# Optimization experiments

Measured on AMD Instinct MI355X. Metric: run time of the kernel, lower is better.

The kernel has to match this reference:

```python
import jax, jax.numpy as jnp
import numpy as np

B, D, A, H, NH = 32768, 768, 17, 128, 4
DH = H // NH


def _ln(x, g, b, eps=1e-5):
    mu = jnp.mean(x, axis=-1, keepdims=True)
    var = jnp.mean((x - mu) ** 2, axis=-1, keepdims=True)
    return (x - mu) / jnp.sqrt(var + eps) * g + b


def setup_inputs() -> dict:
    key = jax.random.key(0)
    ks = jax.random.split(key, 16)
    s = 0.02
    return {
        "visual_feat": jax.random.normal(ks[0], (B, D), jnp.float32),
        "au_feat": jax.random.uniform(ks[1], (B, A), jnp.float32),
        "w_tok": jax.random.normal(ks[2], (H, 1), jnp.float32) * s,
        "b_tok": jnp.zeros((H,), jnp.float32),
        "pos": jax.random.normal(ks[3], (1, A, H), jnp.float32) * s,
        "g_auln": jnp.ones((H,), jnp.float32),
        "b_auln": jnp.zeros((H,), jnp.float32),
        "w_q": jax.random.normal(ks[4], (H, D), jnp.float32) * s,
        "b_q": jnp.zeros((H,), jnp.float32),
        "w_in": jax.random.normal(ks[5], (3 * H, H), jnp.float32) * s,  # packed q,k,v in_proj
        "b_in": jnp.zeros((3 * H,), jnp.float32),
        "w_ao": jax.random.normal(ks[6], (H, H), jnp.float32) * s,  # MHA out_proj
        "b_ao": jnp.zeros((H,), jnp.float32),
        "g_aln": jnp.ones((H,), jnp.float32),
        "b_aln": jnp.zeros((H,), jnp.float32),
        "w_out": jax.random.normal(ks[7], (D, H), jnp.float32) * s,
        "b_out": jnp.zeros((D,), jnp.float32),
        "w_gate": jax.random.normal(ks[8], (D, 2 * D), jnp.float32) * s,
        "b_gate": jnp.zeros((D,), jnp.float32),
    }


def reference(visual_feat, au_feat, w_tok, b_tok, pos, g_auln, b_auln,
              w_q, b_q, w_in, b_in, w_ao, b_ao, g_aln, b_aln,
              w_out, b_out, w_gate, b_gate):
    # AU tokens: Linear(1 -> H) on intensities, + pos embed, LN. [B, A, H]
    au_tokens = au_feat[..., None] * w_tok[:, 0] + b_tok
    au_tokens = _ln(au_tokens + pos, g_auln, b_auln)
    # query: [B, H] (seq len 1)
    query = visual_feat @ w_q.T + b_q
    # MultiheadAttention (batch_first, packed in_proj)
    wq, wk, wv = w_in[:H], w_in[H:2 * H], w_in[2 * H:]
    bq, bk, bv = b_in[:H], b_in[H:2 * H], b_in[2 * H:]
    q = (query @ wq.T + bq).reshape(-1, NH, DH)          # [B, nh, dh]
    k = (au_tokens @ wk.T + bk).reshape(-1, A, NH, DH)   # [B, A, nh, dh]
    v = (au_tokens @ wv.T + bv).reshape(-1, A, NH, DH)
    scale = 1.0 / jnp.sqrt(jnp.asarray(DH, q.dtype))
    scores = jnp.einsum('bhd,bahd->bha', q * scale, k)   # [B, nh, A]
    attn = jax.nn.softmax(scores, axis=-1)
    ctx = jnp.einsum('bha,bahd->bhd', attn, v).reshape(-1, H)
    attn_out = ctx @ w_ao.T + b_ao
    attn_out = _ln(attn_out, g_aln, b_aln)
    attn_feat = attn_out @ w_out.T + b_out               # [B, D]
    gate_in = jnp.concatenate([visual_feat, attn_feat], axis=1)
    gate = jax.nn.sigmoid(gate_in @ w_gate.T + b_gate)
    return gate * attn_feat + (1.0 - gate) * visual_feat
```

## Files before the change

### kernel.cpp

```cpp
#include <hip/hip_runtime.h>
#include <hip/hip_bf16.h>

typedef __hip_bfloat16 bf16;
typedef __attribute__((ext_vector_type(8))) short short8;
typedef __attribute__((ext_vector_type(4))) float f32x4;
typedef __attribute__((ext_vector_type(8))) __bf16 bf16x8;

#define NB 32768
#define DD 768
#define AA 17
#define HH 128

__device__ __forceinline__ float bs2f(short s){
  unsigned int u = ((unsigned int)(unsigned short)s) << 16;
  return __builtin_bit_cast(float, u);
}
__device__ __forceinline__ short f2bs(float f){
  bf16 h = __float2bfloat16(f);
  return __builtin_bit_cast(short, h);
}
__device__ __forceinline__ f32x4 mfma16(short8 a, short8 b, f32x4 c){
  return __builtin_amdgcn_mfma_f32_16x16x32_bf16(
      __builtin_bit_cast(bf16x8, a), __builtin_bit_cast(bf16x8, b), c, 0, 0, 0);
}

template<int F32>
__device__ __forceinline__ short8 ldchunk(const void* base, long elem_off){
  if (F32){
    const float4* p = (const float4*)((const float*)base + elem_off);
    float4 x = p[0], y = p[1];
    short8 r;
    r[0]=f2bs(x.x); r[1]=f2bs(x.y); r[2]=f2bs(x.z); r[3]=f2bs(x.w);
    r[4]=f2bs(y.x); r[5]=f2bs(y.y); r[6]=f2bs(y.z); r[7]=f2bs(y.w);
    return r;
  } else {
    return *(const short8*)((const short*)base + elem_off);
  }
}


__device__ __forceinline__ float blk_mean128(float v, float* tmp){
  int t = threadIdx.x;
  #pragma unroll
  for (int m = 32; m; m >>= 1) v += __shfl_xor(v, m);
  if ((t & 63) == 0) tmp[t >> 6] = v;
  __syncthreads();
  float r = (tmp[0] + tmp[1]) * (1.0f / 128.0f);
  __syncthreads();
  return r;
}

__global__ void prep1(const float* __restrict__ w_tok, const float* __restrict__ b_tok,
                      const float* __restrict__ pos, const float* __restrict__ g_auln,
                      float* __restrict__ ug, float* __restrict__ rg, float* __restrict__ coef){
  __shared__ float tmp[2];
  int h = threadIdx.x;
  float w = w_tok[h];
  float wbar = blk_mean128(w, tmp);
  float u = w - wbar;
  float g = g_auln[h];
  ug[h] = u * g;
  float muu = blk_mean128(u * u, tmp);
  if (h == 0) coef[0] = muu;
  float bt = b_tok[h];
  for (int a = 0; a < AA; ++a){
    float c = bt + pos[a * HH + h];
    float cbar = blk_mean128(c, tmp);
    float r = c - cbar;
    rg[a * HH + h] = r * g;
    float mur = blk_mean128(u * r, tmp);
    float mrr = blk_mean128(r * r, tmp);
    if (h == 0){ coef[1 + a] = mur; coef[18 + a] = mrr; }
  }
}

__global__ void prep2(const float* __restrict__ w_in, const float* __restrict__ b_in,
                      const float* __restrict__ b_auln, const float* __restrict__ b_q,
                      const float* __restrict__ ug, const float* __restrict__ rg,
                      float* __restrict__ Uk, float* __restrict__ Ck,
                      float* __restrict__ Uv, float* __restrict__ Cv,
                      float* __restrict__ Rk, float* __restrict__ Rv,
                      float* __restrict__ bqf){
  int hp = threadIdx.x, bid = blockIdx.x;
  const float* wqrow = w_in + (long)hp * HH;
  const float* wkrow = w_in + (long)(HH + hp) * HH;
  const float* wvrow = w_in + (long)(2 * HH + hp) * HH;
  if (bid < AA){
    int a = bid;
    float sk = 0.f, sv = 0.f;
    for (int t = 0; t < HH; ++t){
      float r = rg[a * HH + t];
      sk += r * wkrow[t];
      sv += r * wvrow[t];
    }
    Rk[a * HH + hp] = sk; Rv[a * HH + hp] = sv;
  } else if (bid == AA){
    float uk = 0.f, uv = 0.f, ck = 0.f, cv = 0.f;
    for (int t = 0; t < HH; ++t){
      float u = ug[t], ba = b_auln[t];
      float wk = wkrow[t], wv = wvrow[t];
      uk += u * wk; uv += u * wv; ck += ba * wk; cv += ba * wv;
    }
    Uk[hp] = uk; Uv[hp] = uv;
    Ck[hp] = ck + b_in[HH + hp];
    Cv[hp] = cv + b_in[2 * HH + hp];
  } else {
    float s = 0.f;
    for (int t = 0; t < HH; ++t) s += b_q[t] * wqrow[t];
    bqf[hp] = s + b_in[hp];
  }
}

__global__ void prep_wqf(const float* __restrict__ w_in, const float* __restrict__ w_q,
                         bf16* __restrict__ Wqf){
  __shared__ float wq[HH];
  int h = blockIdx.x, t = threadIdx.x;
  if (t < HH) wq[t] = w_in[(long)h * HH + t];
  __syncthreads();
  for (int j = t; j < DD; j += 256){
    float acc = 0.f;
    for (int k = 0; k < HH; ++k) acc += wq[k] * w_q[(long)k * DD + j];
    Wqf[(long)h * DD + j] = __float2bfloat16(acc);
  }
}

__global__ void prep_gate(const float* __restrict__ w_gate, const float* __restrict__ b_gate,
                          const float* __restrict__ w_out, const float* __restrict__ b_out,
                          bf16* __restrict__ Wg1b, bf16* __restrict__ Wg2w,
                          bf16* __restrict__ Woutb, float* __restrict__ bgp){
  __shared__ float wg2[DD];
  __shared__ float red[2];
  int c = blockIdx.x, t = threadIdx.x;
  const float* wrow = w_gate + (long)c * (2 * DD);
  for (int j = t; j < DD; j += 128){
    Wg1b[(long)c * DD + j] = __float2bfloat16(wrow[j]);
    wg2[j] = wrow[DD + j];
  }
  __syncthreads();
  float acc = 0.f;
  for (int j = 0; j < DD; ++j) acc = fmaf(wg2[j], w_out[(long)j * HH + t], acc);
  Wg2w[(long)c * HH + t] = __float2bfloat16(acc);
  Woutb[(long)c * HH + t] = __float2bfloat16(w_out[(long)c * HH + t]);
  float pb = 0.f;
  for (int j = t; j < DD; j += 128) pb = fmaf(wg2[j], b_out[j], pb);
  #pragma unroll
  for (int m = 32; m; m >>= 1) pb += __shfl_xor(pb, m);
  if ((t & 63) == 0) red[t >> 6] = pb;
  __syncthreads();
  if (t == 0) bgp[c] = b_gate[c] + red[0] + red[1];
}

__global__ __launch_bounds__(128) void attn(
    const bf16* __restrict__ Q, const float* __restrict__ au, const float* __restrict__ coef,
    const float* __restrict__ Uk_, const float* __restrict__ Ck_,
    const float* __restrict__ Uv_, const float* __restrict__ Cv_,
    const float* __restrict__ Rk, const float* __restrict__ Rv,
    bf16* __restrict__ ctx){
  const int ROWS = 8;
  int h = threadIdx.x;
  long row0 = (long)blockIdx.x * ROWS;
  float Uk = Uk_[h], Ck = Ck_[h], Uv = Uv_[h], Cv = Cv_[h];
  float cA = coef[0];
  __shared__ float sa[ROWS * AA];
  for (int idx = h; idx < ROWS * AA; idx += 128)
    sa[idx] = au[row0 * AA + idx];
  __syncthreads();
  const float scale = 0.17677669529663689f;
  for (int r = 0; r < ROWS; ++r){
    long row = row0 + r;
    float q = __bfloat162float(Q[row * HH + h]);
    float sc[AA], vv[AA];
    #pragma unroll
    for (int a = 0; a < AA; ++a){
      float s = sa[r * AA + a];
      float var = fmaf(s * s, cA, fmaf(2.f * s, coef[1 + a], coef[18 + a]));
      float rinv = rsqrtf(fmaxf(var, 0.f) + 1e-5f);
      float kk = fmaf(s, Uk, Rk[a * HH + h]) * rinv + Ck;
      vv[a]    = fmaf(s, Uv, Rv[a * HH + h]) * rinv + Cv;
      float p = q * kk;
      p += __shfl_xor(p, 16); p += __shfl_xor(p, 8); p += __shfl_xor(p, 4);
      p += __shfl_xor(p, 2);  p += __shfl_xor(p, 1);
      sc[a] = p * scale;
    }
    float mx = sc[0];
    #pragma unroll
    for (int a = 1; a < AA; ++a) mx = fmaxf(mx, sc[a]);
    float den = 0.f, cval = 0.f;
    #pragma unroll
    for (int a = 0; a < AA; ++a){
      float e = __expf(sc[a] - mx);
      den += e; cval += e * vv[a];
    }
    ctx[row * HH + h] = __float2bfloat16(cval / den);
  }
}

template<int MODE, int AF, int BF, int SIDE>
__global__ __launch_bounds__(256) void gemm_bt(
    const void* __restrict__ A, long lda, int ks,
    const void* __restrict__ Bw, long ldb,
    const float* __restrict__ bias,
    const float* __restrict__ g_ln, const float* __restrict__ b_ln,
    short* __restrict__ sideA,
    bf16* __restrict__ C, long ldc)
{
  __shared__ __align__(16) short smem[20480];
  const int tid = threadIdx.x;
  const int w = tid >> 6, l = tid & 63;
  const long rowBase = (long)blockIdx.y * 128;
  const int colBase = blockIdx.x * 128;
  const int fr = l & 15;
  const int kq = l >> 4;
  const int sr0 = tid >> 2,         sp0 = (tid & 3) * 8;
  const int sr1 = (tid + 256) >> 2;

  f32x4 acc[2][8];
  f32x4 zero = {0.f, 0.f, 0.f, 0.f};
  #pragma unroll
  for (int i = 0; i < 2; ++i)
    #pragma unroll
    for (int j = 0; j < 8; ++j) acc[i][j] = zero;

  {
    short8 av0 = ldchunk<AF>(A, (rowBase + sr0) * lda + sp0);
    short8 av1 = ldchunk<AF>(A, (rowBase + sr1) * lda + sp0);
    short8 bv0 = ldchunk<BF>(Bw, (long)(colBase + sr0) * ldb + sp0);
    short8 bv1 = ldchunk<BF>(Bw, (long)(colBase + sr1) * ldb + sp0);
    if (SIDE){
      *(short8*)(sideA + (rowBase + sr0) * lda + sp0) = av0;
      *(short8*)(sideA + (rowBase + sr1) * lda + sp0) = av1;
    }
    *(short8*)(smem + sr0 * 40 + sp0) = av0;
    *(short8*)(smem + sr1 * 40 + sp0) = av1;
    *(short8*)(smem + 5120 + sr0 * 40 + sp0) = bv0;
    *(short8*)(smem + 5120 + sr1 * 40 + sp0) = bv1;
  }

  for (int kt = 0; kt < ks; ++kt){
    __syncthreads();
    short* cb = smem + (kt & 1) * 10240;
    short* nb = smem + ((kt + 1) & 1) * 10240;
    const bool pf = (kt + 1 < ks);
    short8 av0, av1, bv0, bv1;
    if (pf){
      const long kA = (long)(kt + 1) * 32;
      av0 = ldchunk<AF>(A, (rowBase + sr0) * lda + kA + sp0);
      av1 = ldchunk<AF>(A, (rowBase + sr1) * lda + kA + sp0);
      bv0 = ldchunk<BF>(Bw, (long)(colBase + sr0) * ldb + kA + sp0);
      bv1 = ldchunk<BF>(Bw, (long)(colBase + sr1) * ldb + kA + sp0);
      if (SIDE){
        *(short8*)(sideA + (rowBase + sr0) * lda + kA + sp0) = av0;
        *(short8*)(sideA + (rowBase + sr1) * lda + kA + sp0) = av1;
      }
    }
    const int ra0 = w * 32 + fr;
    short8 a0 = *(const short8*)(cb + ra0 * 40 + kq * 8);
    short8 a1 = *(const short8*)(cb + (ra0 + 16) * 40 + kq * 8);
    #pragma unroll
    for (int nt = 0; nt < 8; ++nt){
      short8 b = *(const short8*)(cb + 5120 + (nt * 16 + fr) * 40 + kq * 8);
      acc[0][nt] = mfma16(a0, b, acc[0][nt]);
      acc[1][nt] = mfma16(a1, b, acc[1][nt]);
    }
    if (pf){
      *(short8*)(nb + sr0 * 40 + sp0) = av0;
      *(short8*)(nb + sr1 * 40 + sp0) = av1;
      *(short8*)(nb + 5120 + sr0 * 40 + sp0) = bv0;
      *(short8*)(nb + 5120 + sr1 * 40 + sp0) = bv1;
    }
  }
  __syncthreads();

  short* ep = smem;
  if (MODE == 1){
    #pragma unroll
    for (int mt = 0; mt < 2; ++mt){
      #pragma unroll
      for (int r = 0; r < 4; ++r){
        float x[8]; float sm = 0.f, sq = 0.f;
        #pragma unroll
        for (int nt = 0; nt < 8; ++nt){
          const int col = colBase + nt * 16 + fr;
          x[nt] = acc[mt][nt][r] + bias[col];
          sm += x[nt]; sq += x[nt] * x[nt];
        }
        sm += __shfl_xor(sm, 1); sq += __shfl_xor(sq, 1);
        sm += __shfl_xor(sm, 2); sq += __shfl_xor(sq, 2);
        sm += __shfl_xor(sm, 4); sq += __shfl_xor(sq, 4);
        sm += __shfl_xor(sm, 8); sq += __shfl_xor(sq, 8);
        const float mu = sm * (1.f / 128.f);
        const float var = sq * (1.f / 128.f) - mu * mu;
        const float rinv = rsqrtf(fmaxf(var, 0.f) + 1e-5f);
        const int lrow = w * 32 + mt * 16 + kq * 4 + r;
        #pragma unroll
        for (int nt = 0; nt < 8; ++nt){
          const int col = colBase + nt * 16 + fr;
          float y = (x[nt] - mu) * rinv * g_ln[col] + b_ln[col];
          ep[lrow * 136 + nt * 16 + fr] = f2bs(y);
        }
      }
    }
  } else {
    #pragma unroll
    for (int nt = 0; nt < 8; ++nt){
      const int col = colBase + nt * 16 + fr;
      const float bv = bias[col];
      #pragma unroll
      for (int mt = 0; mt < 2; ++mt){
        const int lrow0 = w * 32 + mt * 16 + kq * 4;
        #pragma unroll
        for (int r = 0; r < 4; ++r)
          ep[(lrow0 + r) * 136 + nt * 16 + fr] = f2bs(acc[mt][nt][r] + bv);
      }
    }
  }
  __syncthreads();

  #pragma unroll
  for (int it = 0; it < 8; ++it){
    const int cid = tid + it * 256;
    const int rw = cid >> 4;
    const int cc = (cid & 15) * 8;
    const long gr = rowBase + rw;
    short8 vls = *(const short8*)(ep + rw * 136 + cc);
    short* cp = (short*)C + gr * ldc + colBase + cc;
    *(short8*)cp = vls;
  }
}

template<int A1F>
__global__ __launch_bounds__(256) void gemm_final(
    const void* __restrict__ A1,
    const bf16* __restrict__ aon,
    const bf16* __restrict__ Wg1b,
    const bf16* __restrict__ Wg2w,
    const bf16* __restrict__ Woutb,
    const float* __restrict__ bgp,
    const float* __restrict__ b_out,
    const float* __restrict__ vf,
    float* __restrict__ C)
{
  __shared__ __align__(16) short smem[20480];
  const int tid = threadIdx.x;
  const int w = tid >> 6, l = tid & 63;

  const int nx = 6;
  const int bid = blockIdx.y * nx + blockIdx.x;
  const int cpx = (NB / 128) * nx / 8;
  const int swz = (bid & 7) * cpx + (bid >> 3);
  const long rowBase = (long)(swz / nx) * 128;
  const int colBase = (swz % nx) * 128;

  const int fr = l & 15;
  const int kq = l >> 4;
  const int sr0 = tid >> 2,         sp0 = (tid & 3) * 8;
  const int sr1 = (tid + 256) >> 2;

  f32x4 accG[2][8], accF[2][8];
  f32x4 zero = {0.f, 0.f, 0.f, 0.f};
  #pragma unroll
  for (int i = 0; i < 2; ++i)
    #pragma unroll
    for (int j = 0; j < 8; ++j){ accG[i][j] = zero; accF[i][j] = zero; }

  {
    short8 av0 = ldchunk<A1F>(A1, (rowBase + sr0) * DD + sp0);
    short8 av1 = ldchunk<A1F>(A1, (rowBase + sr1) * DD + sp0);
    short8 bv0 = *(const short8*)((const short*)Wg1b + (long)(colBase + sr0) * DD + sp0);
    short8 bv1 = *(const short8*)((const short*)Wg1b + (long)(colBase + sr1) * DD + sp0);
    *(short8*)(smem + sr0 * 40 + sp0) = av0;
    *(short8*)(smem + sr1 * 40 + sp0) = av1;
    *(short8*)(smem + 5120 + sr0 * 40 + sp0) = bv0;
    *(short8*)(smem + 5120 + sr1 * 40 + sp0) = bv1;
  }
  for (int kt = 0; kt < DD / 32; ++kt){
    __syncthreads();
    short* cb = smem + (kt & 1) * 10240;
    short* nb = smem + ((kt + 1) & 1) * 10240;
    const bool pf = (kt + 1 < DD / 32);
    short8 av0, av1, bv0, bv1;
    if (pf){
      const long kA = (long)(kt + 1) * 32;
      av0 = ldchunk<A1F>(A1, (rowBase + sr0) * DD + kA + sp0);
      av1 = ldchunk<A1F>(A1, (rowBase + sr1) * DD + kA + sp0);
      bv0 = *(const short8*)((const short*)Wg1b + (long)(colBase + sr0) * DD + kA + sp0);
      bv1 = *(const short8*)((const short*)Wg1b + (long)(colBase + sr1) * DD + kA + sp0);
    }
    const int ra0 = w * 32 + fr;
    short8 a0 = *(const short8*)(cb + ra0 * 40 + kq * 8);
    short8 a1 = *(const short8*)(cb + (ra0 + 16) * 40 + kq * 8);
    #pragma unroll
    for (int nt = 0; nt < 8; ++nt){
      short8 b = *(const short8*)(cb + 5120 + (nt * 16 + fr) * 40 + kq * 8);
      accG[0][nt] = mfma16(a0, b, accG[0][nt]);
      accG[1][nt] = mfma16(a1, b, accG[1][nt]);
    }
    if (pf){
      *(short8*)(nb + sr0 * 40 + sp0) = av0;
      *(short8*)(nb + sr1 * 40 + sp0) = av1;
      *(short8*)(nb + 5120 + sr0 * 40 + sp0) = bv0;
      *(short8*)(nb + 5120 + sr1 * 40 + sp0) = bv1;
    }
  }

  short* As = smem;
  short* Bs = smem + 5120;
  short* Bs2 = smem + 10240;
  for (int kt = 0; kt < HH / 32; ++kt){
    const long kA = (long)kt * 32;
    short8 av0 = *(const short8*)((const short*)aon + (rowBase + sr0) * HH + kA + sp0);
    short8 av1 = *(const short8*)((const short*)aon + (rowBase + sr1) * HH + kA + sp0);
    short8 bv0 = *(const short8*)((const short*)Wg2w + (long)(colBase + sr0) * HH + kA + sp0);
    short8 bv1 = *(const short8*)((const short*)Wg2w + (long)(colBase + sr1) * HH + kA + sp0);
    short8 cv0 = *(const short8*)((const short*)Woutb + (long)(colBase + sr0) * HH + kA + sp0);
    short8 cv1 = *(const short8*)((const short*)Woutb + (long)(colBase + sr1) * HH + kA + sp0);
    __syncthreads();
    *(short8*)(As + sr0 * 40 + sp0) = av0;
    *(short8*)(As + sr1 * 40 + sp0) = av1;
    *(short8*)(Bs + sr0 * 40 + sp0) = bv0;
    *(short8*)(Bs + sr1 * 40 + sp0) = bv1;
    *(short8*)(Bs2 + sr0 * 40 + sp0) = cv0;
    *(short8*)(Bs2 + sr1 * 40 + sp0) = cv1;
    __syncthreads();
    const int ra0 = w * 32 + fr;
    short8 a0 = *(const short8*)(As + ra0 * 40 + kq * 8);
    short8 a1 = *(const short8*)(As + (ra0 + 16) * 40 + kq * 8);
    #pragma unroll
    for (int nt = 0; nt < 8; ++nt){
      short8 b  = *(const short8*)(Bs  + (nt * 16 + fr) * 40 + kq * 8);
      short8 b2 = *(const short8*)(Bs2 + (nt * 16 + fr) * 40 + kq * 8);
      accG[0][nt] = mfma16(a0, b,  accG[0][nt]);
      accG[1][nt] = mfma16(a1, b,  accG[1][nt]);
      accF[0][nt] = mfma16(a0, b2, accF[0][nt]);
      accF[1][nt] = mfma16(a1, b2, accF[1][nt]);
    }
  }

  float bg[8], bo[8];
  #pragma unroll
  for (int nt = 0; nt < 8; ++nt){
    const int col = colBase + nt * 16 + fr;
    bg[nt] = bgp[col];
    bo[nt] = b_out[col];
  }
  #pragma unroll
  for (int mt = 0; mt < 2; ++mt){
    const long r0 = rowBase + w * 32 + mt * 16 + kq * 4;
    #pragma unroll
    for (int r = 0; r < 4; ++r){
      const long row = r0 + r;
      const float* vrow = vf + row * DD;
      float* crow = C + row * DD;
      #pragma unroll
      for (int nt = 0; nt < 8; ++nt){
        const int col = colBase + nt * 16 + fr;
        const float lin = accG[mt][nt][r] + bg[nt];
        const float afv = accF[mt][nt][r] + bo[nt];
        const float gate = 1.f / (1.f + __expf(-lin));
        crow[col] = gate * afv + (1.f - gate) * vrow[col];
      }
    }
  }
}

extern "C" void kernel_launch(void* const* d_in, const int* in_sizes, int n_in,
                              void* d_out, int out_size, void* d_ws, size_t ws_size,
                              hipStream_t stream){
  const float* visual = (const float*)d_in[0];
  const float* au     = (const float*)d_in[1];
  const float* w_tok  = (const float*)d_in[2];
  const float* b_tok  = (const float*)d_in[3];
  const float* pos    = (const float*)d_in[4];
  const float* g_auln = (const float*)d_in[5];
  const float* b_auln = (const float*)d_in[6];
  const float* w_q    = (const float*)d_in[7];
  const float* b_q    = (const float*)d_in[8];
  const float* w_in   = (const float*)d_in[9];
  const float* b_in   = (const float*)d_in[10];
  const float* w_ao   = (const float*)d_in[11];
  const float* b_ao   = (const float*)d_in[12];
  const float* g_aln  = (const float*)d_in[13];
  const float* b_aln  = (const float*)d_in[14];
  const float* w_out  = (const float*)d_in[15];
  const float* b_out  = (const float*)d_in[16];
  const float* w_gate = (const float*)d_in[17];
  const float* b_gate = (const float*)d_in[18];

  char* ob = (char*)d_out;
  bf16* Q   = (bf16*)(ob);
  bf16* ctx = (bf16*)(ob + ((size_t)8 << 20));
  char* p = ob + ((size_t)16 << 20);
  auto alloc = [&](size_t bytes){ char* r = p; p += (bytes + 255) & ~(size_t)255; return r; };
  bf16*  Wqf  = (bf16*) alloc((size_t)HH * DD * 2);
  float* bqf  = (float*)alloc(HH * 4);
  float* ug   = (float*)alloc(HH * 4);
  float* rg   = (float*)alloc(AA * HH * 4);
  float* coef = (float*)alloc(64 * 4);
  float* Uk   = (float*)alloc(HH * 4);
  float* Ck   = (float*)alloc(HH * 4);
  float* Uv   = (float*)alloc(HH * 4);
  float* Cv   = (float*)alloc(HH * 4);
  float* Rk   = (float*)alloc(AA * HH * 4);
  float* Rv   = (float*)alloc(AA * HH * 4);

  char* q = (char*)d_ws;
  auto walloc = [&](size_t bytes){ char* r = q; q += (bytes + 255) & ~(size_t)255; return r; };
  bf16*  aon   = (bf16*) walloc((size_t)NB * HH * 2);
  bf16*  Wg1b  = (bf16*) walloc((size_t)DD * DD * 2);
  bf16*  Wg2w  = (bf16*) walloc((size_t)DD * HH * 2);
  bf16*  Woutb = (bf16*) walloc((size_t)DD * HH * 2);
  float* bgp   = (float*)walloc(DD * 4);
  bf16*  vbf   = (bf16*) walloc((size_t)NB * DD * 2);
  const bool use_vbf = (size_t)(q - (char*)d_ws) <= ws_size;

  prep1<<<dim3(1), dim3(128), 0, stream>>>(w_tok, b_tok, pos, g_auln, ug, rg, coef);
  prep2<<<dim3(19), dim3(128), 0, stream>>>(w_in, b_in, b_auln, b_q, ug, rg, Uk, Ck, Uv, Cv, Rk, Rv, bqf);
  prep_wqf<<<dim3(128), dim3(256), 0, stream>>>(w_in, w_q, Wqf);
  prep_gate<<<dim3(DD), dim3(128), 0, stream>>>(w_gate, b_gate, w_out, b_out, Wg1b, Wg2w, Woutb, bgp);

  if (use_vbf)
    gemm_bt<0, 1, 0, 1><<<dim3(1, NB / 128), dim3(256), 0, stream>>>(
        visual, (long)DD, DD / 32, Wqf, (long)DD,
        bqf, nullptr, nullptr, (short*)vbf, Q, (long)HH);
  else
    gemm_bt<0, 1, 0, 0><<<dim3(1, NB / 128), dim3(256), 0, stream>>>(
        visual, (long)DD, DD / 32, Wqf, (long)DD,
        bqf, nullptr, nullptr, nullptr, Q, (long)HH);

  attn<<<dim3(NB / 8), dim3(128), 0, stream>>>(Q, au, coef, Uk, Ck, Uv, Cv, Rk, Rv, ctx);

  gemm_bt<1, 0, 1, 0><<<dim3(1, NB / 128), dim3(256), 0, stream>>>(
      ctx, (long)HH, HH / 32, w_ao, (long)HH,
      b_ao, g_aln, b_aln, nullptr, aon, (long)HH);

  if (use_vbf)
    gemm_final<0><<<dim3(DD / 128, NB / 128), dim3(256), 0, stream>>>(
        vbf, aon, Wg1b, Wg2w, Woutb, bgp, b_out, visual, (float*)d_out);
  else
    gemm_final<1><<<dim3(DD / 128, NB / 128), dim3(256), 0, stream>>>(
        visual, aon, Wg1b, Wg2w, Woutb, bgp, b_out, visual, (float*)d_out);
}
```

Before: 578.0 us.

## Stage gate GEMM tiles via global_load_lds with XOR-swizzled shared layout

In the final gated GEMM, the bf16 path now loads A and weight tiles straight from global memory into LDS with global_load_lds, double-buffered. This drops the register round-trip and the padded layout, and an XOR swizzle on the 16-byte chunks is meant to avoid bank conflicts. The fp32-input path switches to a single-buffered swizzled layout. The intent is to cut VGPR pressure, instruction count and LDS usage, which may raise occupancy. The risk is that the async-copy synchronisation relies only on __syncthreads before the next tile is read.

```diff
diff --git a/kernel.cpp b/kernel.cpp
--- a/kernel.cpp
+++ b/kernel.cpp
@@ -5,6 +5,8 @@
 typedef __attribute__((ext_vector_type(8))) short short8;
 typedef __attribute__((ext_vector_type(4))) float f32x4;
 typedef __attribute__((ext_vector_type(8))) __bf16 bf16x8;
+typedef const __attribute__((address_space(1))) void* gas_ptr;
+typedef __attribute__((address_space(3))) void* las_ptr;
 
 #define NB 32768
 #define DD 768
@@ -22,6 +24,9 @@
 __device__ __forceinline__ f32x4 mfma16(short8 a, short8 b, f32x4 c){
   return __builtin_amdgcn_mfma_f32_16x16x32_bf16(
       __builtin_bit_cast(bf16x8, a), __builtin_bit_cast(bf16x8, b), c, 0, 0, 0);
+}
+__device__ __forceinline__ void glds16(const short* g, short* l){
+  __builtin_amdgcn_global_load_lds((gas_ptr)g, (las_ptr)l, 16, 0, 0);
 }
 
 template<int F32>
@@ -340,9 +345,9 @@
     const float* __restrict__ vf,
     float* __restrict__ C)
 {
-  __shared__ __align__(16) short smem[20480];
+  __shared__ __align__(16) short smem[16384];
   const int tid = threadIdx.x;
-  const int w = tid >> 6, l = tid & 63;
+  const int wv = tid >> 6, l = tid & 63;
 
   const int nx = 6;
   const int bid = blockIdx.y * nx + blockIdx.x;
@@ -353,8 +358,7 @@
 
   const int fr = l & 15;
   const int kq = l >> 4;
-  const int sr0 = tid >> 2,         sp0 = (tid & 3) * 8;
-  const int sr1 = (tid + 256) >> 2;
+  const int swofs = ((kq ^ ((l >> 1) & 3)) << 3);
 
   f32x4 accG[2][8], accF[2][8];
   f32x4 zero = {0.f, 0.f, 0.f, 0.f};
@@ -363,76 +367,102 @@
     #pragma unroll
     for (int j = 0; j < 8; ++j){ accG[i][j] = zero; accF[i][j] = zero; }
 
+  if (A1F == 0){
+    const short* Ab = (const short*)A1;
+    const short* Bb = (const short*)Wg1b;
+    const int srow = l >> 2;
+    const int schunk = ((l & 3) ^ ((l >> 3) & 3)) * 8;
+    #define STAGE_P1(p, kt) {                                                        \
+      short* dA = smem + (p) * 8192;                                                 \
+      _Pragma("unroll")                                                              \
+      for (int i = 0; i < 2; ++i){                                                   \
+        const int r = wv * 32 + i * 16 + srow;                                       \
+        glds16(Ab + ((rowBase + r) * (long)DD + (kt) * 32 + schunk),                 \
+               dA + wv * 1024 + i * 512);                                            \
+        glds16(Bb + ((long)(colBase + r) * DD + (kt) * 32 + schunk),                 \
+               dA + 4096 + wv * 1024 + i * 512);                                     \
+      }                                                                              \
+    }
+    STAGE_P1(0, 0);
+    for (int kt = 0; kt < DD / 32; ++kt){
+      __syncthreads();
+      if (kt + 1 < DD / 32) STAGE_P1((kt + 1) & 1, kt + 1);
+      short* cb = smem + (kt & 1) * 8192;
+      const int ra0 = wv * 32 + fr;
+      short8 a0 = *(const short8*)(cb + ra0 * 32 + swofs);
+      short8 a1 = *(const short8*)(cb + (ra0 + 16) * 32 + swofs);
+      #pragma unroll
+      for (int nt = 0; nt < 8; ++nt){
+        short8 b = *(const short8*)(cb + 4096 + (nt * 16 + fr) * 32 + swofs);
+        accG[0][nt] = mfma16(a0, b, accG[0][nt]);
+        accG[1][nt] = mfma16(a1, b, accG[1][nt]);
+      }
+    }
+    #undef STAGE_P1
+  } else {
+    const int sr0 = tid >> 2, sc = tid & 3;
+    const int sr1 = sr0 + 64;
+    const int sp = sc * 8;
+    const int ss0 = (sc ^ ((sr0 >> 1) & 3)) * 8;
+    const int ss1 = (sc ^ ((sr1 >> 1) & 3)) * 8;
+    for (int kt = 0; kt < DD / 32; ++kt){
+      const long kA = (long)kt * 32;
+      short8 av0 = ldchunk<1>(A1, (rowBase + sr0) * (long)DD + kA + sp);
+      short8 av1 = ldchunk<1>(A1, (rowBase + sr1) * (long)DD + kA + sp);
+      short8 bv0 = *(const short8*)((const short*)Wg1b + (long)(colBase + sr0) * DD + kA + sp);
+      short8 bv1 = *(const short8*)((const short*)Wg1b + (long)(colBase + sr1) * DD + kA + sp);
+      __syncthreads();
+      *(short8*)(smem + sr0 * 32 + ss0) = av0;
+      *(short8*)(smem + sr1 * 32 + ss1) = av1;
+      *(short8*)(smem + 4096 + sr0 * 32 + ss0) = bv0;
+      *(short8*)(smem + 4096 + sr1 * 32 + ss1) = bv1;
+      __syncthreads();
+      const int ra0 = wv * 32 + fr;
+      short8 a0 = *(const short8*)(smem + ra0 * 32 + swofs);
+      short8 a1 = *(const short8*)(smem + (ra0 + 16) * 32 + swofs);
+      #pragma unroll
+      for (int nt = 0; nt < 8; ++nt){
+        short8 b = *(const short8*)(smem + 4096 + (nt * 16 + fr) * 32 + swofs);
+        accG[0][nt] = mfma16(a0, b, accG[0][nt]);
+        accG[1][nt] = mfma16(a1, b, accG[1][nt]);
+      }
+    }
+  }
+
   {
-    short8 av0 = ldchunk<A1F>(A1, (rowBase + sr0) * DD + sp0);
-    short8 av1 = ldchunk<A1F>(A1, (rowBase + sr1) * DD + sp0);
-    short8 bv0 = *(const short8*)((const short*)Wg1b + (long)(colBase + sr0) * DD + sp0);
-    short8 bv1 = *(const short8*)((const short*)Wg1b + (long)(colBase + sr1) * DD + sp0);
-    *(short8*)(smem + sr0 * 40 + sp0) = av0;
-    *(short8*)(smem + sr1 * 40 + sp0) = av1;
-    *(short8*)(smem + 5120 + sr0 * 40 + sp0) = bv0;
-    *(short8*)(smem + 5120 + sr1 * 40 + sp0) = bv1;
-  }
-  for (int kt = 0; kt < DD / 32; ++kt){
-    __syncthreads();
-    short* cb = smem + (kt & 1) * 10240;
-    short* nb = smem + ((kt + 1) & 1) * 10240;
-    const bool pf = (kt + 1 < DD / 32);
-    short8 av0, av1, bv0, bv1;
-    if (pf){
-      const long kA = (long)(kt + 1) * 32;
-      av0 = ldchunk<A1F>(A1, (rowBase + sr0) * DD + kA + sp0);
-      av1 = ldchunk<A1F>(A1, (rowBase + sr1) * DD + kA + sp0);
-      bv0 = *(const short8*)((const short*)Wg1b + (long)(colBase + sr0) * DD + kA + sp0);
-      bv1 = *(const short8*)((const short*)Wg1b + (long)(colBase + sr1) * DD + kA + sp0);
-    }
-    const int ra0 = w * 32 + fr;
-    short8 a0 = *(const short8*)(cb + ra0 * 40 + kq * 8);
-    short8 a1 = *(const short8*)(cb + (ra0 + 16) * 40 + kq * 8);
-    #pragma unroll
-    for (int nt = 0; nt < 8; ++nt){
-      short8 b = *(const short8*)(cb + 5120 + (nt * 16 + fr) * 40 + kq * 8);
-      accG[0][nt] = mfma16(a0, b, accG[0][nt]);
-      accG[1][nt] = mfma16(a1, b, accG[1][nt]);
-    }
-    if (pf){
-      *(short8*)(nb + sr0 * 40 + sp0) = av0;
-      *(short8*)(nb + sr1 * 40 + sp0) = av1;
-      *(short8*)(nb + 5120 + sr0 * 40 + sp0) = bv0;
-      *(short8*)(nb + 5120 + sr1 * 40 + sp0) = bv1;
-    }
-  }
-
-  short* As = smem;
-  short* Bs = smem + 5120;
-  short* Bs2 = smem + 10240;
-  for (int kt = 0; kt < HH / 32; ++kt){
-    const long kA = (long)kt * 32;
-    short8 av0 = *(const short8*)((const short*)aon + (rowBase + sr0) * HH + kA + sp0);
-    short8 av1 = *(const short8*)((const short*)aon + (rowBase + sr1) * HH + kA + sp0);
-    short8 bv0 = *(const short8*)((const short*)Wg2w + (long)(colBase + sr0) * HH + kA + sp0);
-    short8 bv1 = *(const short8*)((const short*)Wg2w + (long)(colBase + sr1) * HH + kA + sp0);
-    short8 cv0 = *(const short8*)((const short*)Woutb + (long)(colBase + sr0) * HH + kA + sp0);
-    short8 cv1 = *(const short8*)((const short*)Woutb + (long)(colBase + sr1) * HH + kA + sp0);
-    __syncthreads();
-    *(short8*)(As + sr0 * 40 + sp0) = av0;
-    *(short8*)(As + sr1 * 40 + sp0) = av1;
-    *(short8*)(Bs + sr0 * 40 + sp0) = bv0;
-    *(short8*)(Bs + sr1 * 40 + sp0) = bv1;
-    *(short8*)(Bs2 + sr0 * 40 + sp0) = cv0;
-    *(short8*)(Bs2 + sr1 * 40 + sp0) = cv1;
-    __syncthreads();
-    const int ra0 = w * 32 + fr;
-    short8 a0 = *(const short8*)(As + ra0 * 40 + kq * 8);
-    short8 a1 = *(const short8*)(As + (ra0 + 16) * 40 + kq * 8);
-    #pragma unroll
-    for (int nt = 0; nt < 8; ++nt){
-      short8 b  = *(const short8*)(Bs  + (nt * 16 + fr) * 40 + kq * 8);
-      short8 b2 = *(const short8*)(Bs2 + (nt * 16 + fr) * 40 + kq * 8);
-      accG[0][nt] = mfma16(a0, b,  accG[0][nt]);
-      accG[1][nt] = mfma16(a1, b,  accG[1][nt]);
-      accF[0][nt] = mfma16(a0, b2, accF[0][nt]);
-      accF[1][nt] = mfma16(a1, b2, accF[1][nt]);
+    short* As = smem;
+    short* Bs = smem + 5120;
+    short* Bs2 = smem + 10240;
+    const int sr0 = tid >> 2, sp0 = (tid & 3) * 8;
+    const int sr1 = sr0 + 64;
+    for (int kt = 0; kt < HH / 32; ++kt){
+      const long kA = (long)kt * 32;
+      short8 av0 = *(const short8*)((const short*)aon + (rowBase + sr0) * HH + kA + sp0);
+      short8 av1 = *(const short8*)((const short*)aon + (rowBase + sr1) * HH + kA + sp0);
+      short8 bv0 = *(const short8*)((const short*)Wg2w + (long)(colBase + sr0) * HH + kA + sp0);
+      short8 bv1 = *(const short8*)((const short*)Wg2w + (long)(colBase + sr1) * HH + kA + sp0);
+      short8 cv0 = *(const short8*)((const short*)Woutb + (long)(colBase + sr0) * HH + kA + sp0);
+      short8 cv1 = *(const short8*)((const short*)Woutb + (long)(colBase + sr1) * HH + kA + sp0);
+      __syncthreads();
+      *(short8*)(As + sr0 * 40 + sp0) = av0;
+      *(short8*)(As + sr1 * 40 + sp0) = av1;
+      *(short8*)(Bs + sr0 * 40 + sp0) = bv0;
+      *(short8*)(Bs + sr1 * 40 + sp0) = bv1;
+      *(short8*)(Bs2 + sr0 * 40 + sp0) = cv0;
+      *(short8*)(Bs2 + sr1 * 40 + sp0) = cv1;
+      __syncthreads();
+      const int ra0 = wv * 32 + fr;
+      short8 a0 = *(const short8*)(As + ra0 * 40 + kq * 8);
+      short8 a1 = *(const short8*)(As + (ra0 + 16) * 40 + kq * 8);
+      #pragma unroll
+      for (int nt = 0; nt < 8; ++nt){
+        short8 b  = *(const short8*)(Bs  + (nt * 16 + fr) * 40 + kq * 8);
+        short8 b2 = *(const short8*)(Bs2 + (nt * 16 + fr) * 40 + kq * 8);
+        accG[0][nt] = mfma16(a0, b,  accG[0][nt]);
+        accG[1][nt] = mfma16(a1, b,  accG[1][nt]);
+        accF[0][nt] = mfma16(a0, b2, accF[0][nt]);
+        accF[1][nt] = mfma16(a1, b2, accF[1][nt]);
+      }
     }
   }
 
@@ -445,7 +475,7 @@
   }
   #pragma unroll
   for (int mt = 0; mt < 2; ++mt){
-    const long r0 = rowBase + w * 32 + mt * 16 + kq * 4;
+    const long r0 = rowBase + wv * 32 + mt * 16 + kq * 4;
     #pragma unroll
     for (int r = 0; r < 4; ++r){
       const long row = r0 + r;
```

After: 498.0 us. 1.16x faster.
